# Kernel tuning notes

Measured on AMD Instinct MI355X. Metric: run time of the kernel, lower is better.

## Reference

```python
import jax, jax.numpy as jnp
import numpy as np
import math

DIM = 1024
NUM_HEADS = 16
HEAD_DIM = DIM // NUM_HEADS
ROPE_BASE = 10000.0


def _rope_cos_sin(seq_len, head_dim, dtype):
    inv_freq = 1.0 / (ROPE_BASE ** (jnp.arange(0, head_dim, 2, dtype=jnp.float32) / head_dim))
    t = jnp.arange(seq_len, dtype=jnp.float32)
    freqs = jnp.einsum('i,j->ij', t, inv_freq)          # (S, head_dim/2)
    emb = jnp.concatenate([freqs, freqs], axis=-1)      # (S, head_dim)
    return jnp.cos(emb).astype(dtype), jnp.sin(emb).astype(dtype)


def _rotate_half(x):
    x1, x2 = jnp.split(x, 2, axis=-1)
    return jnp.concatenate([-x2, x1], axis=-1)


def setup_inputs() -> dict:
    key = jax.random.key(0)
    kx, kq, kk, kv, ko = jax.random.split(key, 5)
    B, S = 4, 2048
    scale = 1.0 / math.sqrt(DIM)
    x = jax.random.normal(kx, (B, S, DIM), dtype=jnp.float32)
    Wq = jax.random.normal(kq, (DIM, DIM), dtype=jnp.float32) * scale
    Wk = jax.random.normal(kk, (DIM, DIM), dtype=jnp.float32) * scale
    Wv = jax.random.normal(kv, (DIM, DIM), dtype=jnp.float32) * scale
    Wo = jax.random.normal(ko, (DIM, DIM), dtype=jnp.float32) * scale
    mask = jnp.tril(jnp.ones((S, S), dtype=jnp.int32))  # causal mask
    return {"x": x, "Wq": Wq, "Wk": Wk, "Wv": Wv, "Wo": Wo, "mask": mask}


def reference(x, Wq, Wk, Wv, Wo, mask):
    B, S, _ = x.shape
    # projections (nn.Linear: y = x @ W.T)
    def split_heads(t):
        return t.reshape(B, S, NUM_HEADS, HEAD_DIM).transpose(0, 2, 1, 3)  # (B,H,S,D)
    q = split_heads(x @ Wq.T)
    k = split_heads(x @ Wk.T)
    v = split_heads(x @ Wv.T)
    # RoPE
    cos, sin = _rope_cos_sin(S, HEAD_DIM, x.dtype)      # (S, D)
    cos = cos[None, None]; sin = sin[None, None]
    q = q * cos + _rotate_half(q) * sin
    k = k * cos + _rotate_half(k) * sin
    # attention
    scores = jnp.einsum('bhsd,bhtd->bhst', q, k) / math.sqrt(HEAD_DIM)
    neg_inf = jnp.asarray(-jnp.inf, dtype=scores.dtype)
    scores = jnp.where(mask[None, None] == 0, neg_inf, scores)
    attn = jax.nn.softmax(scores, axis=-1)
    out = jnp.einsum('bhst,bhtd->bhsd', attn, v)        # (B,H,S,D)
    out = out.transpose(0, 2, 1, 3).reshape(B, S, DIM)
    return out @ Wo.T
```

## Files before the change

kernel.cpp:

```cpp
#include <hip/hip_runtime.h>
#include <hip/hip_bf16.h>

#define BDIM 1024
#define NH 16
#define HD 64
#define BB 4
#define SS 2048
#define MTOT (BB*SS)
#define NT (SS/64)

typedef __bf16 bf16x8 __attribute__((ext_vector_type(8)));
typedef float f32x4 __attribute__((ext_vector_type(4)));

__device__ __forceinline__ unsigned short f2b(float f){
    union { float f; unsigned u; } v; v.f = f;
    unsigned r = v.u + 0x7fffu + ((v.u >> 16) & 1u);
    return (unsigned short)(r >> 16);
}
__device__ __forceinline__ float b2f(unsigned short h){
    union { unsigned u; float f; } v; v.u = ((unsigned)h) << 16;
    return v.f;
}

__device__ __forceinline__ void ld16(const unsigned short* g, unsigned short* l){
    __builtin_amdgcn_global_load_lds(
        (const __attribute__((address_space(1))) unsigned int*)(const void*)g,
        (__attribute__((address_space(3))) unsigned int*)(void*)l, 16, 0, 0);
}

__global__ void convert_f32_bf16(const float* __restrict__ in,
                                 unsigned short* __restrict__ out, int n4){
    int i = blockIdx.x * blockDim.x + threadIdx.x;
    if (i < n4){
        float4 v = ((const float4*)in)[i];
        ushort4 o;
        o.x = f2b(v.x); o.y = f2b(v.y); o.z = f2b(v.z); o.w = f2b(v.w);
        ((ushort4*)out)[i] = o;
    }
}

__global__ void convert_weights(const float* __restrict__ Wq, const float* __restrict__ Wk,
                                const float* __restrict__ Wv, const float* __restrict__ Wo,
                                unsigned short* __restrict__ oq, unsigned short* __restrict__ ok,
                                unsigned short* __restrict__ ov, unsigned short* __restrict__ oo){
    const float* in = (blockIdx.y == 0) ? Wq : (blockIdx.y == 1) ? Wk : (blockIdx.y == 2) ? Wv : Wo;
    unsigned short* out = (blockIdx.y == 0) ? oq : (blockIdx.y == 1) ? ok : (blockIdx.y == 2) ? ov : oo;
    int i = blockIdx.x * blockDim.x + threadIdx.x;
    float4 v = ((const float4*)in)[i];
    ushort4 o;
    o.x = f2b(v.x); o.y = f2b(v.y); o.z = f2b(v.z); o.w = f2b(v.w);
    ((ushort4*)out)[i] = o;
}

__device__ __forceinline__ void gemm_mainloop(
    const unsigned short* __restrict__ A,
    const unsigned short* __restrict__ Bw,
    unsigned short* At, unsigned short* Bt,
    f32x4 acc[4][4], int m0, int n0)
{
    const int tid  = threadIdx.x;
    const int lane = tid & 63;
    const int wave = tid >> 6;
    const int wr = wave >> 1, wc = wave & 1;
    const int lh = lane >> 4, ll = lane & 15;
    const int K = 1024;

    for (int k0 = 0; k0 < K; k0 += 64){
        #pragma unroll
        for (int c = 0; c < 4; ++c){
            int g   = c*256 + tid;
            int row = g >> 3;
            int off = (g & 7) * 8;
            int base = (c*256 + wave*64) * 8;
            ld16(A  + (size_t)(m0+row)*K + k0 + off, At + base);
            ld16(Bw + (size_t)(n0+row)*K + k0 + off, Bt + base);
        }
        __syncthreads();
        #pragma unroll
        for (int ks = 0; ks < 2; ++ks){
            bf16x8 af[4], bfr[4];
            #pragma unroll
            for (int i = 0; i < 4; ++i)
                af[i] = *(const bf16x8*)(At + (wr*64 + i*16 + ll)*64 + ks*32 + lh*8);
            #pragma unroll
            for (int j = 0; j < 4; ++j)
                bfr[j] = *(const bf16x8*)(Bt + (wc*64 + j*16 + ll)*64 + ks*32 + lh*8);
            #pragma unroll
            for (int i = 0; i < 4; ++i)
                #pragma unroll
                for (int j = 0; j < 4; ++j)
                    acc[i][j] = __builtin_amdgcn_mfma_f32_16x16x32_bf16(af[i], bfr[j], acc[i][j], 0, 0, 0);
        }
        __syncthreads();
    }
}

__global__ __launch_bounds__(256, 2) void gemm_qkv(
    const unsigned short* __restrict__ Xb,
    const unsigned short* __restrict__ Wq,
    const unsigned short* __restrict__ Wk,
    const unsigned short* __restrict__ Wv,
    unsigned short* __restrict__ Qt,
    unsigned short* __restrict__ Kt,
    unsigned short* __restrict__ VTt)
{
    __shared__ alignas(16) unsigned short At[128*64];
    __shared__ alignas(16) unsigned short Bt[128*64];
    const int z = blockIdx.z;
    const unsigned short* Bw = (z == 0) ? Wq : (z == 1 ? Wk : Wv);
    const int m0 = blockIdx.y * 128, n0 = blockIdx.x * 128;
    f32x4 acc[4][4] = {};
    gemm_mainloop(Xb, Bw, At, Bt, acc, m0, n0);

    const int lane = threadIdx.x & 63;
    const int wave = threadIdx.x >> 6;
    const int wr = wave >> 1, wc = wave & 1;
    const int lh = lane >> 4, ll = lane & 15;
    const int h  = blockIdx.x*2 + wc;
    const int b  = m0 >> 11;

    if (z < 2){
        const float qs = (z == 0) ? 0.125f * 1.44269504f : 1.0f;
        unsigned short* C = (z == 0) ? Qt : Kt;
        #pragma unroll
        for (int i = 0; i < 4; ++i)
            #pragma unroll
            for (int r = 0; r < 4; ++r){
                int m = m0 + wr*64 + i*16 + lh*4 + r;
                int s = m & (SS-1);
                size_t base = (((size_t)(b*NH + h)*SS + s) << 6);
                #pragma unroll
                for (int jl = 0; jl < 2; ++jl){
                    int d_lo = jl*16 + ll;
                    float theta = (float)s * exp2f(-0.41524101186092029f * (float)d_lo);
                    float sn, c;
                    sincosf(theta, &sn, &c);
                    float a_lo = acc[i][jl][r], a_hi = acc[i][jl+2][r];
                    float y_lo = (a_lo*c - a_hi*sn) * qs;
                    float y_hi = (a_hi*c + a_lo*sn) * qs;
                    C[base + d_lo]      = f2b(y_lo);
                    C[base + d_lo + 32] = f2b(y_hi);
                }
            }
    } else {
        const int s0 = (m0 & (SS-1)) + wr*64;
        #pragma unroll
        for (int i = 0; i < 4; ++i)
            #pragma unroll
            for (int j = 0; j < 4; ++j){
                int d = j*16 + ll;
                unsigned short tmp[4];
                #pragma unroll
                for (int r = 0; r < 4; ++r)
                    tmp[r] = f2b(acc[i][j][r]);
                size_t off = ((size_t)(b*NH + h)*HD + d)*SS + s0 + i*16 + lh*4;
                *(uint2*)(VTt + off) = *(const uint2*)tmp;
            }
    }
}

__global__ __launch_bounds__(256, 2) void gemm_out(
    const unsigned short* __restrict__ Ab,
    const unsigned short* __restrict__ Wo,
    float* __restrict__ Cout)
{
    __shared__ alignas(16) unsigned short At[128*64];
    __shared__ alignas(16) unsigned short Bt[128*64];
    const int m0 = blockIdx.y * 128, n0 = blockIdx.x * 128;
    f32x4 acc[4][4] = {};
    gemm_mainloop(Ab, Wo, At, Bt, acc, m0, n0);

    const int lane = threadIdx.x & 63;
    const int wave = threadIdx.x >> 6;
    const int wr = wave >> 1, wc = wave & 1;
    const int lh = lane >> 4, ll = lane & 15;
    #pragma unroll
    for (int i = 0; i < 4; ++i)
        #pragma unroll
        for (int j = 0; j < 4; ++j)
            #pragma unroll
            for (int r = 0; r < 4; ++r){
                int m = m0 + wr*64 + i*16 + lh*4 + r;
                int n = n0 + wc*64 + j*16 + ll;
                Cout[(size_t)m*BDIM + n] = acc[i][j][r];
            }
}

__device__ __forceinline__ void attn_tile(
    const bf16x8 qf[2], bool diag, int ws, int lh, int ll,
    const unsigned short* Ksh, const unsigned short* Vsh, unsigned short* Prow,
    float li[4], f32x4 o[4])
{
    f32x4 sc[4] = {};
    #pragma unroll
    for (int ks = 0; ks < 2; ++ks)
        #pragma unroll
        for (int j = 0; j < 4; ++j){
            bf16x8 bfr = *(const bf16x8*)(Ksh + (j*16 + ll)*72 + ks*32 + lh*8);
            sc[j] = __builtin_amdgcn_mfma_f32_16x16x32_bf16(qf[ks], bfr, sc[j], 0, 0, 0);
        }
    if (diag){
        #pragma unroll
        for (int j = 0; j < 4; ++j){
            int key = j*16 + ll;
            #pragma unroll
            for (int r = 0; r < 4; ++r){
                int qrow = ws*16 + lh*4 + r;
                if (key > qrow) sc[j][r] = -1e30f;
            }
        }
    }
    #pragma unroll
    for (int j = 0; j < 4; ++j)
        #pragma unroll
        for (int r = 0; r < 4; ++r)
            sc[j][r] = exp2f(sc[j][r] - 28.0f);
    #pragma unroll
    for (int r = 0; r < 4; ++r)
        li[r] += (sc[0][r] + sc[1][r]) + (sc[2][r] + sc[3][r]);
    #pragma unroll
    for (int j = 0; j < 4; ++j)
        #pragma unroll
        for (int r = 0; r < 4; ++r)
            Prow[(lh*4 + r)*72 + j*16 + ll] = f2b(sc[j][r]);
    #pragma unroll
    for (int ks = 0; ks < 2; ++ks){
        bf16x8 pf = *(const bf16x8*)(Prow + ll*72 + ks*32 + lh*8);
        #pragma unroll
        for (int t = 0; t < 4; ++t){
            bf16x8 vf = *(const bf16x8*)(Vsh + (t*16 + ll)*72 + ks*32 + lh*8);
            o[t] = __builtin_amdgcn_mfma_f32_16x16x32_bf16(pf, vf, o[t], 0, 0, 0);
        }
    }
}

__device__ __forceinline__ void store_o(
    unsigned short* S, const f32x4 o[4], const float li[4],
    int lane, int lh, int ll, int q0w, int b, int h,
    unsigned short* __restrict__ Obuf)
{
    #pragma unroll
    for (int r = 0; r < 4; ++r){
        float inv = 1.0f / li[r];
        #pragma unroll
        for (int t = 0; t < 4; ++t)
            S[(lh*4 + r)*72 + t*16 + ll] = f2b(o[t][r] * inv);
    }
    int row = lane >> 2, c4 = (lane & 3) * 8;
    size_t rb = ((size_t)(b*SS + q0w + row))*BDIM + h*HD;
    *(uint4*)(Obuf + rb + c4)      = *(uint4*)(S + row*72 + c4);
    *(uint4*)(Obuf + rb + 32 + c4) = *(uint4*)(S + row*72 + 32 + c4);
}

__global__ __launch_bounds__(512, 4) void attn_kernel(
    const unsigned short* __restrict__ Qt,
    const unsigned short* __restrict__ Kt,
    const unsigned short* __restrict__ VTt,
    unsigned short* __restrict__ Obuf)
{
    __shared__ alignas(16) unsigned short Ksh[64*72];
    __shared__ alignas(16) unsigned short Vsh[64*72];
    __shared__ alignas(16) unsigned short Psh[8][16*72];

    const int tid  = threadIdx.x;
    const int lane = tid & 63;
    const int wave = tid >> 6;
    const int grp  = wave >> 2;
    const int ws   = wave & 3;
    const int lh = lane >> 4, ll = lane & 15;
    const int bx = blockIdx.x;
    const int bh = blockIdx.y;

    const int tS = (grp == 0) ? bx        : 15 - bx;
    const int tL = (grp == 0) ? NT-1 - bx : 16 + bx;
    const int ktMax = NT-1 - bx;

    const unsigned short* Qh  = Qt  + (size_t)bh * SS * HD;
    const unsigned short* Kh  = Kt  + (size_t)bh * SS * HD;
    const unsigned short* VTh = VTt + (size_t)bh * HD * SS;

    bf16x8 qfS[2], qfL[2];
    {
        int qrS = tS*64 + ws*16 + ll;
        int qrL = tL*64 + ws*16 + ll;
        #pragma unroll
        for (int ks = 0; ks < 2; ++ks){
            qfS[ks] = *(const bf16x8*)(Qh + (size_t)qrS*HD + ks*32 + lh*8);
            qfL[ks] = *(const bf16x8*)(Qh + (size_t)qrL*HD + ks*32 + lh*8);
        }
    }

    f32x4 oS[4] = {}, oL[4] = {};
    float liS[4] = {0.f,0.f,0.f,0.f}, liL[4] = {0.f,0.f,0.f,0.f};

    const int srow = tid >> 3;
    const int soff = (tid & 7) * 8;

    uint4 kr = *(const uint4*)(Kh  + (size_t)srow*HD + soff);
    uint4 vr = *(const uint4*)(VTh + (size_t)srow*SS + soff);

    for (int kt = 0; kt <= ktMax; ++kt){
        __syncthreads();
        *(uint4*)(Ksh + srow*72 + soff) = kr;
        *(uint4*)(Vsh + srow*72 + soff) = vr;
        __syncthreads();
        if (kt < ktMax){
            int t0n = (kt + 1) * 64;
            kr = *(const uint4*)(Kh  + (size_t)(t0n + srow)*HD + soff);
            vr = *(const uint4*)(VTh + (size_t)srow*SS + t0n + soff);
        }
        if (kt <= tL)
            attn_tile(qfL, kt == tL, ws, lh, ll, Ksh, Vsh, Psh[wave], liL, oL);
        if (kt <= tS)
            attn_tile(qfS, kt == tS, ws, lh, ll, Ksh, Vsh, Psh[wave], liS, oS);
    }

    #pragma unroll
    for (int r = 0; r < 4; ++r){
        float sS = liS[r], sL = liL[r];
        #pragma unroll
        for (int x = 1; x < 16; x <<= 1){
            sS += __shfl_xor(sS, x);
            sL += __shfl_xor(sL, x);
        }
        liS[r] = sS; liL[r] = sL;
    }

    int b = bh >> 4, h = bh & 15;
    store_o(Psh[wave], oS, liS, lane, lh, ll, tS*64 + ws*16, b, h, Obuf);
    store_o(Psh[wave], oL, liL, lane, lh, ll, tL*64 + ws*16, b, h, Obuf);
}

extern "C" void kernel_launch(void* const* d_in, const int* in_sizes, int n_in,
                              void* d_out, int out_size, void* d_ws, size_t ws_size,
                              hipStream_t stream) {
    const float* x  = (const float*)d_in[0];
    const float* Wq = (const float*)d_in[1];
    const float* Wk = (const float*)d_in[2];
    const float* Wv = (const float*)d_in[3];
    const float* Wo = (const float*)d_in[4];

    char* w = (char*)d_ws;
    unsigned short* xb  = (unsigned short*)(w);
    unsigned short* wqb = (unsigned short*)(w + (16u  << 20));
    unsigned short* wkb = (unsigned short*)(w + (18u  << 20));
    unsigned short* wvb = (unsigned short*)(w + (20u  << 20));
    unsigned short* wob = (unsigned short*)(w + (22u  << 20));
    unsigned short* Qt  = (unsigned short*)(w + (24u  << 20));
    unsigned short* Kt  = (unsigned short*)(w + (40u  << 20));
    unsigned short* VTt = (unsigned short*)(w + (56u  << 20));
    unsigned short* Ob  = (unsigned short*)(w + (72u  << 20));

    convert_f32_bf16<<<8192, 256, 0, stream>>>(x, xb, 2097152);
    convert_weights<<<dim3(1024, 4), 256, 0, stream>>>(Wq, Wk, Wv, Wo, wqb, wkb, wvb, wob);

    gemm_qkv<<<dim3(8, 64, 3), 256, 0, stream>>>(xb, wqb, wkb, wvb, Qt, Kt, VTt);
    attn_kernel<<<dim3(8, 64), 512, 0, stream>>>(Qt, Kt, VTt, Ob);
    gemm_out<<<dim3(8, 64), 256, 0, stream>>>(Ob, wob, (float*)d_out);
}
```

Measured before the change: 288.5 us.

## Swizzle GEMM LDS layout and enlarge QKV tile to 256 rows with 512 threads

Adds an XOR swizzle to the LDS tile layout on both the global-to-LDS load and the fragment read, to avoid bank conflicts in the MFMA operand loads. The QKV projection GEMM now uses 512-thread blocks covering 256 rows of X, so each weight tile is shared by twice as many rows. Launch bounds change to (512, 6). The out-projection keeps its 128x128 tile but picks up the swizzle. In the QKV epilogue, wr = wave>>1 now spans 0..3 over 256 rows, which appears consistent with the new tile.

```diff
diff --git a/kernel.cpp b/kernel.cpp
--- a/kernel.cpp
+++ b/kernel.cpp
@@ -52,6 +52,7 @@
     ((ushort4*)out)[i] = o;
 }
 
+template<int NTHR, int MROWS>
 __device__ __forceinline__ void gemm_mainloop(
     const unsigned short* __restrict__ A,
     const unsigned short* __restrict__ Bw,
@@ -64,27 +65,34 @@
     const int wr = wave >> 1, wc = wave & 1;
     const int lh = lane >> 4, ll = lane & 15;
     const int K = 1024;
+    const int soff = ((lane & 7) ^ ((lane >> 3) & 7)) * 8;
+    const int ch0  = ((    lh) ^ (ll & 7)) * 8;
+    const int ch1  = ((4 + lh) ^ (ll & 7)) * 8;
 
     for (int k0 = 0; k0 < K; k0 += 64){
         #pragma unroll
-        for (int c = 0; c < 4; ++c){
-            int g   = c*256 + tid;
-            int row = g >> 3;
-            int off = (g & 7) * 8;
-            int base = (c*256 + wave*64) * 8;
-            ld16(A  + (size_t)(m0+row)*K + k0 + off, At + base);
-            ld16(Bw + (size_t)(n0+row)*K + k0 + off, Bt + base);
+        for (int c = 0; c < MROWS*8/NTHR; ++c){
+            int row  = (c*NTHR + tid) >> 3;
+            int base = (c*NTHR + wave*64) * 8;
+            ld16(A + (size_t)(m0+row)*K + k0 + soff, At + base);
+        }
+        #pragma unroll
+        for (int c = 0; c < 128*8/NTHR; ++c){
+            int row  = (c*NTHR + tid) >> 3;
+            int base = (c*NTHR + wave*64) * 8;
+            ld16(Bw + (size_t)(n0+row)*K + k0 + soff, Bt + base);
         }
         __syncthreads();
         #pragma unroll
         for (int ks = 0; ks < 2; ++ks){
+            const int chv = ks ? ch1 : ch0;
             bf16x8 af[4], bfr[4];
             #pragma unroll
             for (int i = 0; i < 4; ++i)
-                af[i] = *(const bf16x8*)(At + (wr*64 + i*16 + ll)*64 + ks*32 + lh*8);
+                af[i] = *(const bf16x8*)(At + (wr*64 + i*16 + ll)*64 + chv);
             #pragma unroll
             for (int j = 0; j < 4; ++j)
-                bfr[j] = *(const bf16x8*)(Bt + (wc*64 + j*16 + ll)*64 + ks*32 + lh*8);
+                bfr[j] = *(const bf16x8*)(Bt + (wc*64 + j*16 + ll)*64 + chv);
             #pragma unroll
             for (int i = 0; i < 4; ++i)
                 #pragma unroll
@@ -95,7 +103,7 @@
     }
 }
 
-__global__ __launch_bounds__(256, 2) void gemm_qkv(
+__global__ __launch_bounds__(512, 6) void gemm_qkv(
     const unsigned short* __restrict__ Xb,
     const unsigned short* __restrict__ Wq,
     const unsigned short* __restrict__ Wk,
@@ -104,13 +112,13 @@
     unsigned short* __restrict__ Kt,
     unsigned short* __restrict__ VTt)
 {
-    __shared__ alignas(16) unsigned short At[128*64];
+    __shared__ alignas(16) unsigned short At[256*64];
     __shared__ alignas(16) unsigned short Bt[128*64];
     const int z = blockIdx.z;
     const unsigned short* Bw = (z == 0) ? Wq : (z == 1 ? Wk : Wv);
-    const int m0 = blockIdx.y * 128, n0 = blockIdx.x * 128;
+    const int m0 = blockIdx.y * 256, n0 = blockIdx.x * 128;
     f32x4 acc[4][4] = {};
-    gemm_mainloop(Xb, Bw, At, Bt, acc, m0, n0);
+    gemm_mainloop<512, 256>(Xb, Bw, At, Bt, acc, m0, n0);
 
     const int lane = threadIdx.x & 63;
     const int wave = threadIdx.x >> 6;
@@ -168,7 +176,7 @@
     __shared__ alignas(16) unsigned short Bt[128*64];
     const int m0 = blockIdx.y * 128, n0 = blockIdx.x * 128;
     f32x4 acc[4][4] = {};
-    gemm_mainloop(Ab, Wo, At, Bt, acc, m0, n0);
+    gemm_mainloop<256, 128>(Ab, Wo, At, Bt, acc, m0, n0);
 
     const int lane = threadIdx.x & 63;
     const int wave = threadIdx.x >> 6;
@@ -354,7 +362,7 @@
     convert_f32_bf16<<<8192, 256, 0, stream>>>(x, xb, 2097152);
     convert_weights<<<dim3(1024, 4), 256, 0, stream>>>(Wq, Wk, Wv, Wo, wqb, wkb, wvb, wob);
 
-    gemm_qkv<<<dim3(8, 64, 3), 256, 0, stream>>>(xb, wqb, wkb, wvb, Qt, Kt, VTt);
+    gemm_qkv<<<dim3(8, 32, 3), 512, 0, stream>>>(xb, wqb, wkb, wvb, Qt, Kt, VTt);
     attn_kernel<<<dim3(8, 64), 512, 0, stream>>>(Qt, Kt, VTt, Ob);
     gemm_out<<<dim3(8, 64), 256, 0, stream>>>(Ob, wob, (float*)d_out);
 }
```

After: 752.3 us. +160.8%, slower.
